# Optimization experiments

Measured on AMD Instinct MI355X. Metric: run time of the kernel, lower is better.

The kernel has to match this reference:

```python
import jax, jax.numpy as jnp
import numpy as np

D_MODEL = 1024
D_STATE = 64
D_HEAD = 64
N_HEADS = 16
D_INNER = D_HEAD * N_HEADS  # 1024
K = 4  # conv kernel size
BATCH = 4
SEQ = 4096
LN_EPS = 1e-5


def setup_inputs() -> dict:
    key = jax.random.key(0)
    k0, k1, k2, k3, k4 = jax.random.split(key, 5)
    x = jax.random.normal(k0, (BATCH, SEQ, D_MODEL), jnp.float32)
    # nn.Linear(d_model, 2*d_inner + 2*d_state, bias=False): weight (out, in)
    in_proj_w = jax.random.normal(k1, (2 * D_INNER + 2 * D_STATE, D_MODEL), jnp.float32) / np.sqrt(D_MODEL).astype(np.float32)
    # depthwise Conv1d: weight (d_inner, 1, K), bias (d_inner,)
    conv_w = jax.random.normal(k2, (D_INNER, 1, K), jnp.float32) * 0.5
    conv_b = jax.random.normal(k3, (D_INNER,), jnp.float32) * 0.1
    # _init_parameters: A = -log(arange(1..d_state)) broadcast to (H, Dh, N)
    A_param = jnp.broadcast_to(-jnp.log(jnp.arange(1, D_STATE + 1, dtype=jnp.float32))[None, None, :],
                               (N_HEADS, D_HEAD, D_STATE))
    ln_w = jnp.ones((D_INNER,), jnp.float32)
    ln_b = jnp.zeros((D_INNER,), jnp.float32)
    out_proj_w = jax.random.normal(k4, (D_MODEL, D_INNER), jnp.float32) / np.sqrt(D_INNER).astype(np.float32)
    return {"x": x, "in_proj_w": in_proj_w, "conv_w": conv_w, "conv_b": conv_b,
            "A_param": A_param, "ln_w": ln_w, "ln_b": ln_b, "out_proj_w": out_proj_w}


def _ssd_scan(xh, Bm, Cm, A_param):
    # xh: (B, L, H, Dh); Bm, Cm: (B, L, N)
    A_disc = jnp.exp(-jnp.exp(A_param))  # (H, Dh, N)

    def step(h, inp):
        x_t, B_t, C_t = inp  # (B,H,Dh), (B,N), (B,N)
        h = h * A_disc + B_t[:, None, None, :] * x_t[..., None]  # (B,H,Dh,N)
        y_t = jnp.einsum('bhdn,bn->bhd', h, C_t)
        return h, y_t

    b = xh.shape[0]
    h0 = jnp.zeros((b, N_HEADS, D_HEAD, D_STATE), xh.dtype)
    xs = (jnp.swapaxes(xh, 0, 1), jnp.swapaxes(Bm, 0, 1), jnp.swapaxes(Cm, 0, 1))
    _, ys = jax.lax.scan(step, h0, xs)  # ys: (L, B, H, Dh)
    return jnp.swapaxes(ys, 0, 1)  # (B, L, H, Dh)


def reference(x, in_proj_w, conv_w, conv_b, A_param, ln_w, ln_b, out_proj_w):
    b, L, _ = x.shape
    xBC = x @ in_proj_w.T  # (B, L, 2*d_inner + 2*d_state)
    xc = xBC[..., :D_INNER]
    z = xBC[..., D_INNER:2 * D_INNER]
    Bm = xBC[..., 2 * D_INNER:2 * D_INNER + D_STATE]
    Cm = xBC[..., 2 * D_INNER + D_STATE:]
    # causal depthwise conv (padding=3 then truncate == left-pad K-1)
    xt = jnp.swapaxes(xc, 1, 2)  # (B, C, L)
    y = jax.lax.conv_general_dilated(xt, conv_w, window_strides=(1,), padding=[(K - 1, 0)],
                                     feature_group_count=D_INNER,
                                     dimension_numbers=('NCH', 'OIH', 'NCH'))
    xc = jnp.swapaxes(y + conv_b[None, :, None], 1, 2)  # (B, L, d_inner)
    xc = jax.nn.silu(xc)
    xh = xc.reshape(b, L, N_HEADS, D_HEAD)
    yssd = _ssd_scan(xh, Bm, Cm, A_param).reshape(b, L, D_INNER)
    yg = yssd * jax.nn.silu(z)
    mu = yg.mean(-1, keepdims=True)
    var = yg.var(-1, keepdims=True)
    yn = (yg - mu) / jnp.sqrt(var + LN_EPS) * ln_w + ln_b
    return yn @ out_proj_w.T
```

## Files before the change

### kernel.cpp

```cpp
#include <hip/hip_runtime.h>

typedef unsigned short u16;
typedef unsigned int u32;
typedef __attribute__((ext_vector_type(8))) short bf16x8;
typedef __attribute__((ext_vector_type(4))) float f32x4;

#define BATCH 4
#define SEQ 4096
#define DMODEL 1024
#define DINNER 1024
#define NPROJ 2176
#define MROWS (BATCH*SEQ)
#define NCHUNK 64
#define CLEN 64
#define NPAD 2304

__device__ __forceinline__ float bf2f(u16 u) {
    union { u32 i; float f; } v; v.i = ((u32)u) << 16; return v.f;
}
__device__ __forceinline__ u16 f2bf(float f) {
    union { float f; u32 i; } v; v.f = f;
    u32 r = v.i + 0x7FFFu + ((v.i >> 16) & 1u);
    return (u16)(r >> 16);
}
__device__ __forceinline__ float silu_f(float x) { return x / (1.0f + expf(-x)); }

__device__ __forceinline__ void gload8f(const u16* p, float* o) {
    bf16x8 v = *(const bf16x8*)p;
    #pragma unroll
    for (int j = 0; j < 8; ++j) o[j] = bf2f((u16)v[j]);
}

__device__ __forceinline__ void ld_lds16(const u16* g, u16* l) {
    __builtin_amdgcn_global_load_lds(
        (const __attribute__((address_space(1))) u32*)g,
        (__attribute__((address_space(3))) u32*)l, 16, 0, 0);
}

__global__ __launch_bounds__(256) void cast_f2b(
    const float* __restrict__ src, u16* __restrict__ dst, int n8)
{
    int i = blockIdx.x * 256 + threadIdx.x;
    if (i >= n8) return;
    size_t o = (size_t)i * 8;
    float4 a = *(const float4*)(src + o);
    float4 b = *(const float4*)(src + o + 4);
    u16 v[8] = {f2bf(a.x), f2bf(a.y), f2bf(a.z), f2bf(a.w),
                f2bf(b.x), f2bf(b.y), f2bf(b.z), f2bf(b.w)};
    *(bf16x8*)(dst + o) = *(bf16x8*)v;
}

__global__ __launch_bounds__(256) void cast_w1p_k(
    const float* __restrict__ src, u16* __restrict__ dst)
{
    int i = blockIdx.x * 256 + threadIdx.x;
    int row = i >> 7;
    size_t o = (size_t)i * 8;
    u16 v[8];
    if (row < NPROJ) {
        float4 a = *(const float4*)(src + o);
        float4 b = *(const float4*)(src + o + 4);
        v[0]=f2bf(a.x); v[1]=f2bf(a.y); v[2]=f2bf(a.z); v[3]=f2bf(a.w);
        v[4]=f2bf(b.x); v[5]=f2bf(b.y); v[6]=f2bf(b.z); v[7]=f2bf(b.w);
    } else {
        #pragma unroll
        for (int j = 0; j < 8; ++j) v[j] = 0;
    }
    *(bf16x8*)(dst + o) = *(bf16x8*)v;
}

__global__ __launch_bounds__(256) void tables_k(
    const float* __restrict__ A_param, float* __restrict__ l2a_g,
    float* __restrict__ apw, float* __restrict__ ainv)
{
    __shared__ float l2s[64];
    int tid = threadIdx.x;
    if (tid < 64) {
        float v = -expf(A_param[tid]) * 1.44269504088896340736f;
        l2s[tid] = v;
        l2a_g[tid] = v;
    }
    __syncthreads();
    #pragma unroll
    for (int i = 0; i < 16; ++i) {
        int e = tid * 16 + i;
        int t = e >> 6, n = e & 63;
        float x = (float)t * l2s[n];
        apw[e]  = exp2f(x);
        ainv[e] = exp2f(-x);
    }
}

#define GK 1024
#define GNT 16

template<typename TO, int GN, int NV, int LDC>
__global__ __launch_bounds__(512, 1) void gemm8p_k(
    const u16* __restrict__ A, const u16* __restrict__ B, TO* __restrict__ C)
{
    __shared__ u16 lds[65536];

    const int cpx = (GN * 64) >> 3;
    const int bid = blockIdx.x;
    const int swz = (bid & 7) * cpx + (bid >> 3);
    const int bm = swz / GN, bn = swz % GN;
    const int m0 = bm * 256, n0 = bn * 256;

    const int tid = threadIdx.x;
    const int wid = tid >> 6, lane = tid & 63;
    const int wm = wid >> 2, wn = wid & 3;
    const int quad = lane >> 4, l16 = lane & 15;
    const int xsw = (l16 & 7) << 3;

    u16* L = lds;
    const u16* Ab = A + (size_t)m0 * GK;
    const u16* Bb = B + (size_t)n0 * GK;

    auto stage = [&](const u16* gbase, u16* ldsb) {
        {
            int c = tid;
            int row = c >> 3, slot = (c & 7) ^ (row & 7);
            ld_lds16(gbase + (size_t)row * GK + slot * 8,
                     ldsb + ((tid & ~63) << 3));
        }
        {
            int c = 512 + tid;
            int row = c >> 3, slot = (c & 7) ^ (row & 7);
            ld_lds16(gbase + (size_t)row * GK + slot * 8,
                     ldsb + ((512 + (tid & ~63)) << 3));
        }
    };
    auto rdfrag = [&](const u16* base, int rh, int kh) -> bf16x8 {
        return *(const bf16x8*)(base + rh * 64 + ((kh * 32 + quad * 8) ^ xsw));
    };

    bf16x8 aLo[4][2], aHi[4][2], bLo[2][2], bHi[2][2];
    f32x4 acc[8][4] = {};

    stage(Ab,                     L);
    stage(Ab + 128 * GK,          L + 8192);
    stage(Bb,                     L + 32768);
    stage(Bb + 128 * GK,          L + 40960);
    stage(Ab + 64,                L + 16384);
    stage(Ab + 128 * GK + 64,     L + 24576);
    asm volatile("s_waitcnt vmcnt(4)" ::: "memory");
    __builtin_amdgcn_s_barrier();
    {
        const u16* Ard = L + wm * 8192;
        #pragma unroll
        for (int i = 0; i < 4; ++i)
            #pragma unroll
            for (int kh = 0; kh < 2; ++kh)
                aLo[i][kh] = rdfrag(Ard, i * 16 + l16, kh);
    }

    for (int t = 0; t < GNT; ++t) {
        const int cb = t & 1;
        u16* Acur = L + cb * 16384;
        u16* Anxt = L + (cb ^ 1) * 16384;
        u16* Bnxt = L + 32768 + (cb ^ 1) * 16384;
        const u16* ArdC = Acur + wm * 8192;
        const u16* ArdN = Anxt + wm * 8192;
        const u16* BrdC = L + 32768 + cb * 16384 + (wn >> 1) * 8192;
        const int brh = (wn & 1) * 64;

        #pragma unroll
        for (int j = 0; j < 2; ++j)
            #pragma unroll
            for (int kh = 0; kh < 2; ++kh)
                bLo[j][kh] = rdfrag(BrdC, brh + j * 16 + l16, kh);
        if (t + 1 < GNT) stage(Bb + (t + 1) * 64, Bnxt);
        __builtin_amdgcn_s_barrier();
        asm volatile("s_waitcnt lgkmcnt(0)" ::: "memory");
        __builtin_amdgcn_s_setprio(1);
        #pragma unroll
        for (int kh = 0; kh < 2; ++kh)
            #pragma unroll
            for (int i = 0; i < 4; ++i)
                #pragma unroll
                for (int j = 0; j < 2; ++j)
                    acc[i][j] = __builtin_amdgcn_mfma_f32_16x16x32_bf16(
                        aLo[i][kh], bLo[j][kh], acc[i][j], 0, 0, 0);
        __builtin_amdgcn_s_setprio(0);
        __builtin_amdgcn_s_barrier();

        #pragma unroll
        for (int j = 0; j < 2; ++j)
            #pragma unroll
            for (int kh = 0; kh < 2; ++kh)
                bHi[j][kh] = rdfrag(BrdC, brh + 32 + j * 16 + l16, kh);
        if (t + 1 < GNT) stage(Bb + 128 * GK + (t + 1) * 64, Bnxt + 8192);
        __builtin_amdgcn_s_barrier();
        asm volatile("s_waitcnt lgkmcnt(0)" ::: "memory");
        __builtin_amdgcn_s_setprio(1);
        #pragma unroll
        for (int kh = 0; kh < 2; ++kh)
            #pragma unroll
            for (int i = 0; i < 4; ++i)
                #pragma unroll
                for (int j = 0; j < 2; ++j)
                    acc[i][2 + j] = __builtin_amdgcn_mfma_f32_16x16x32_bf16(
                        aLo[i][kh], bHi[j][kh], acc[i][2 + j], 0, 0, 0);
        __builtin_amdgcn_s_setprio(0);
        __builtin_amdgcn_s_barrier();

        #pragma unroll
        for (int i = 0; i < 4; ++i)
            #pragma unroll
            for (int kh = 0; kh < 2; ++kh)
                aHi[i][kh] = rdfrag(ArdC, 64 + i * 16 + l16, kh);
        if (t + 2 < GNT) stage(Ab + (t + 2) * 64, Acur);
        if (t + 2 < GNT)      { asm volatile("s_waitcnt vmcnt(6)" ::: "memory"); }
        else if (t + 1 < GNT) { asm volatile("s_waitcnt vmcnt(4)" ::: "memory"); }
        __builtin_amdgcn_s_barrier();
        asm volatile("s_waitcnt lgkmcnt(0)" ::: "memory");
        __builtin_amdgcn_s_setprio(1);
        #pragma unroll
        for (int kh = 0; kh < 2; ++kh)
            #pragma unroll
            for (int i = 0; i < 4; ++i)
                #pragma unroll
                for (int j = 0; j < 2; ++j)
                    acc[4 + i][2 + j] = __builtin_amdgcn_mfma_f32_16x16x32_bf16(
                        aHi[i][kh], bHi[j][kh], acc[4 + i][2 + j], 0, 0, 0);
        __builtin_amdgcn_s_setprio(0);
        __builtin_amdgcn_s_barrier();

        if (t + 1 < GNT) {
            #pragma unroll
            for (int i = 0; i < 4; ++i)
                #pragma unroll
                for (int kh = 0; kh < 2; ++kh)
                    aLo[i][kh] = rdfrag(ArdN, i * 16 + l16, kh);
        }
        if (t + 2 < GNT) stage(Ab + 128 * GK + (t + 2) * 64, Acur + 8192);
        if (t + 2 < GNT)      { asm volatile("s_waitcnt vmcnt(4)" ::: "memory"); }
        else if (t + 1 < GNT) { asm volatile("s_waitcnt vmcnt(0)" ::: "memory"); }
        __builtin_amdgcn_s_barrier();
        asm volatile("s_waitcnt lgkmcnt(0)" ::: "memory");
        __builtin_amdgcn_s_setprio(1);
        #pragma unroll
        for (int kh = 0; kh < 2; ++kh)
            #pragma unroll
            for (int i = 0; i < 4; ++i)
                #pragma unroll
                for (int j = 0; j < 2; ++j)
                    acc[4 + i][j] = __builtin_amdgcn_mfma_f32_16x16x32_bf16(
                        aHi[i][kh], bLo[j][kh], acc[4 + i][j], 0, 0, 0);
        __builtin_amdgcn_s_setprio(0);
        __builtin_amdgcn_s_barrier();
    }

    __syncthreads();
    if constexpr (sizeof(TO) == 2) {
        u16* eld = lds;
        #pragma unroll
        for (int i = 0; i < 8; ++i)
            #pragma unroll
            for (int j = 0; j < 4; ++j)
                #pragma unroll
                for (int r = 0; r < 4; ++r)
                    eld[(size_t)(wm * 128 + i * 16 + quad * 4 + r) * 256 +
                        wn * 64 + j * 16 + l16] = f2bf(acc[i][j][r]);
        __syncthreads();
        #pragma unroll
        for (int rep = 0; rep < 16; ++rep) {
            int cc = rep * 512 + tid;
            int row = cc >> 5, c8 = (cc & 31) * 8;
            if (n0 + c8 < NV)
                *(bf16x8*)(C + (size_t)(m0 + row) * LDC + n0 + c8) =
                    *(const bf16x8*)(eld + (size_t)row * 256 + c8);
        }
    } else {
        float* eldf = (float*)lds;
        #pragma unroll
        for (int h = 0; h < 2; ++h) {
            if (wm == h) {
                #pragma unroll
                for (int i = 0; i < 8; ++i)
                    #pragma unroll
                    for (int j = 0; j < 4; ++j)
                        #pragma unroll
                        for (int r = 0; r < 4; ++r)
                            eldf[(size_t)(i * 16 + quad * 4 + r) * 256 +
                                 wn * 64 + j * 16 + l16] = acc[i][j][r];
            }
            __syncthreads();
            #pragma unroll
            for (int rep = 0; rep < 16; ++rep) {
                int cc = rep * 512 + tid;
                int row = cc >> 6, c4 = (cc & 63) * 4;
                *(float4*)(C + (size_t)(m0 + h * 128 + row) * LDC + n0 + c4) =
                    *(const float4*)(eldf + (size_t)row * 256 + c4);
            }
            __syncthreads();
        }
    }
}

__global__ __launch_bounds__(256) void ssd_intra_k(
    const float* __restrict__ conv_w, const float* __restrict__ conv_b,
    const u16* __restrict__ xBC, u16* __restrict__ yout,
    u16* __restrict__ Sh, const float* __restrict__ apw,
    const float* __restrict__ ainv)
{
    __shared__ u16 Pl[64][72];
    __shared__ u16 Ql[64][72];
    __shared__ u16 Gl[64][72];
    __shared__ u16 Qt[64][72];
    __shared__ u16 Xt[64][72];

    const int dg = blockIdx.x, c = blockIdx.y, b = blockIdx.z;
    const int dcol = dg * 64;
    const int l0 = c * CLEN;
    const int tid = threadIdx.x;
    const int w = tid >> 6, lane = tid & 63;
    const int quad = lane >> 4, l16 = lane & 15;
    const int tstrip = 16 * w;

    {
        const int st_t = tid >> 3, st_n8 = (tid & 7) * 8;
        #pragma unroll
        for (int rep = 0; rep < 2; ++rep) {
            int t = rep * 32 + st_t;
            size_t row = (size_t)(b * SEQ + l0 + t) * NPROJ;
            float Bv[8], Cv[8];
            gload8f(xBC + row + 2048 + st_n8, Bv);
            gload8f(xBC + row + 2112 + st_n8, Cv);
            float4 aw0 = *(const float4*)&apw[t * 64 + st_n8];
            float4 aw1 = *(const float4*)&apw[t * 64 + st_n8 + 4];
            float4 ai0 = *(const float4*)&ainv[t * 64 + st_n8];
            float4 ai1 = *(const float4*)&ainv[t * 64 + st_n8 + 4];
            float4 ar0 = *(const float4*)&apw[(63 - t) * 64 + st_n8];
            float4 ar1 = *(const float4*)&apw[(63 - t) * 64 + st_n8 + 4];
            float aw[8] = {aw0.x,aw0.y,aw0.z,aw0.w,aw1.x,aw1.y,aw1.z,aw1.w};
            float ai[8] = {ai0.x,ai0.y,ai0.z,ai0.w,ai1.x,ai1.y,ai1.z,ai1.w};
            float ar[8] = {ar0.x,ar0.y,ar0.z,ar0.w,ar1.x,ar1.y,ar1.z,ar1.w};
            u16 p8[8], q8[8];
            #pragma unroll
            for (int j = 0; j < 8; ++j) {
                p8[j] = f2bf(Cv[j] * aw[j]);
                q8[j] = f2bf(Bv[j] * ai[j]);
            }
            *(bf16x8*)&Pl[t][st_n8] = *(bf16x8*)p8;
            *(bf16x8*)&Ql[t][st_n8] = *(bf16x8*)q8;
            #pragma unroll
            for (int j = 0; j < 8; ++j)
                Qt[st_n8 + j][t] = f2bf(Bv[j] * ar[j]);
        }
    }
    {
        const int xt_d8 = (tid & 7) * 8;
        const int ch0 = dcol + xt_d8;
        float4 wv[8];
        #pragma unroll
        for (int j = 0; j < 8; ++j)
            wv[j] = *(const float4*)(conv_w + (ch0 + j) * 4);
        float bias[8];
        {
            float4 b0 = *(const float4*)(conv_b + ch0);
            float4 b1 = *(const float4*)(conv_b + ch0 + 4);
            bias[0]=b0.x; bias[1]=b0.y; bias[2]=b0.z; bias[3]=b0.w;
            bias[4]=b1.x; bias[5]=b1.y; bias[6]=b1.z; bias[7]=b1.w;
        }
        #pragma unroll
        for (int rep = 0; rep < 2; ++rep) {
            int xt_t = (tid >> 3) + rep * 32;
            float acc[8];
            #pragma unroll
            for (int j = 0; j < 8; ++j) acc[j] = bias[j];
            #pragma unroll
            for (int k = 0; k < 4; ++k) {
                int lt = l0 + xt_t - 3 + k;
                if (lt < 0) continue;
                float v[8];
                gload8f(xBC + (size_t)(b * SEQ + lt) * NPROJ + ch0, v);
                #pragma unroll
                for (int j = 0; j < 8; ++j) {
                    const float* wj = (const float*)&wv[j];
                    acc[j] += v[j] * wj[k];
                }
            }
            #pragma unroll
            for (int j = 0; j < 8; ++j)
                Xt[xt_d8 + j][xt_t] = f2bf(silu_f(acc[j]));
        }
    }
    __syncthreads();

    bf16x8 af0 = *(const bf16x8*)&Pl[tstrip + l16][0  + quad * 8];
    bf16x8 af1 = *(const bf16x8*)&Pl[tstrip + l16][32 + quad * 8];
    f32x4 g[4] = {};
    #pragma unroll
    for (int j4 = 0; j4 < 4; ++j4) {
        bf16x8 b0 = *(const bf16x8*)&Ql[j4 * 16 + l16][0  + quad * 8];
        bf16x8 b1 = *(const bf16x8*)&Ql[j4 * 16 + l16][32 + quad * 8];
        g[j4] = __builtin_amdgcn_mfma_f32_16x16x32_bf16(af0, b0, g[j4], 0, 0, 0);
        g[j4] = __builtin_amdgcn_mfma_f32_16x16x32_bf16(af1, b1, g[j4], 0, 0, 0);
    }
    __syncthreads();

    #pragma unroll
    for (int j4 = 0; j4 < 4; ++j4) {
        #pragma unroll
        for (int r = 0; r < 4; ++r) {
            int t = tstrip + quad * 4 + r;
            int s = j4 * 16 + l16;
            float val = (s <= t) ? g[j4][r] : 0.f;
            u16 hi = f2bf(val);
            Ql[t][s] = hi;
            Gl[t][s] = f2bf(val - bf2f(hi));
        }
    }
    __syncthreads();

    bf16x8 gh0 = *(const bf16x8*)&Ql[tstrip + l16][0  + quad * 8];
    bf16x8 gh1 = *(const bf16x8*)&Ql[tstrip + l16][32 + quad * 8];
    bf16x8 gl0 = *(const bf16x8*)&Gl[tstrip + l16][0  + quad * 8];
    bf16x8 gl1 = *(const bf16x8*)&Gl[tstrip + l16][32 + quad * 8];
    bf16x8 qt0 = *(const bf16x8*)&Qt[tstrip + l16][0  + quad * 8];
    bf16x8 qt1 = *(const bf16x8*)&Qt[tstrip + l16][32 + quad * 8];

    #pragma unroll
    for (int dt = 0; dt < 4; ++dt) {
        bf16x8 x0 = *(const bf16x8*)&Xt[dt * 16 + l16][0  + quad * 8];
        bf16x8 x1 = *(const bf16x8*)&Xt[dt * 16 + l16][32 + quad * 8];
        f32x4 y = {};
        y = __builtin_amdgcn_mfma_f32_16x16x32_bf16(gh0, x0, y, 0, 0, 0);
        y = __builtin_amdgcn_mfma_f32_16x16x32_bf16(gh1, x1, y, 0, 0, 0);
        y = __builtin_amdgcn_mfma_f32_16x16x32_bf16(gl0, x0, y, 0, 0, 0);
        y = __builtin_amdgcn_mfma_f32_16x16x32_bf16(gl1, x1, y, 0, 0, 0);
        f32x4 s4 = {};
        s4 = __builtin_amdgcn_mfma_f32_16x16x32_bf16(qt0, x0, s4, 0, 0, 0);
        s4 = __builtin_amdgcn_mfma_f32_16x16x32_bf16(qt1, x1, s4, 0, 0, 0);
        #pragma unroll
        for (int r = 0; r < 4; ++r) {
            int t = tstrip + quad * 4 + r;
            yout[(size_t)(b * SEQ + l0 + t) * DINNER + dcol + dt * 16 + l16] = f2bf(y[r]);
            int n = tstrip + quad * 4 + r;
            Sh[((size_t)((b * NCHUNK + c) * 64 + n)) * 1024 + dcol + dt * 16 + l16] = f2bf(s4[r]);
        }
    }
}

__global__ __launch_bounds__(256) void state_scan_k(
    u16* __restrict__ Sh, const float* __restrict__ l2a)
{
    int gid = blockIdx.x * 256 + threadIdx.x;
    int b = gid >> 16, r = gid & 65535, n = r >> 10;
    float a64 = exp2f(64.f * l2a[n]);
    float v = 0.f;
    size_t base = ((size_t)b << 22) + r;
    for (int c = 0; c < NCHUNK; ++c) {
        size_t addr = base + ((size_t)c << 16);
        float s = bf2f(Sh[addr]);
        Sh[addr] = f2bf(v);
        v = fmaf(v, a64, s);
    }
}

__global__ __launch_bounds__(256) void ssd_inter_k(
    u16* __restrict__ Y, const u16* __restrict__ xBC,
    const u16* __restrict__ Sh, const float* __restrict__ apw,
    const float* __restrict__ l2a)
{
    __shared__ u16 Pl[64][72];
    __shared__ u16 Vt[64][72];

    const int dg = blockIdx.x, c = blockIdx.y, b = blockIdx.z;
    const int dcol = dg * 64;
    const int l0 = c * CLEN;
    const int tid = threadIdx.x;
    const int w = tid >> 6, lane = tid & 63;
    const int quad = lane >> 4, l16 = lane & 15;
    const int tstrip = 16 * w;

    {
        const int st_t = tid >> 3, st_n8 = (tid & 7) * 8;
        #pragma unroll
        for (int rep = 0; rep < 2; ++rep) {
            int t = rep * 32 + st_t;
            float Cv[8];
            gload8f(xBC + (size_t)(b * SEQ + l0 + t) * NPROJ + 2112 + st_n8, Cv);
            float4 aw0 = *(const float4*)&apw[t * 64 + st_n8];
            float4 aw1 = *(const float4*)&apw[t * 64 + st_n8 + 4];
            float aw[8] = {aw0.x,aw0.y,aw0.z,aw0.w,aw1.x,aw1.y,aw1.z,aw1.w};
            u16 p8[8];
            #pragma unroll
            for (int j = 0; j < 8; ++j) p8[j] = f2bf(Cv[j] * aw[j]);
            *(bf16x8*)&Pl[t][st_n8] = *(bf16x8*)p8;
        }
    }
    {
        #pragma unroll
        for (int rep = 0; rep < 2; ++rep) {
            int idx = rep * 256 + tid;
            int vn = idx >> 3, vd8 = (idx & 7) * 8;
            float an = exp2f(l2a[vn]);
            bf16x8 vv = *(const bf16x8*)&Sh[((size_t)((b * NCHUNK + c) * 64 + vn)) * 1024 + dcol + vd8];
            #pragma unroll
            for (int j = 0; j < 8; ++j) Vt[vd8 + j][vn] = f2bf(an * bf2f((u16)vv[j]));
        }
    }
    __syncthreads();

    bf16x8 af0 = *(const bf16x8*)&Pl[tstrip + l16][0  + quad * 8];
    bf16x8 af1 = *(const bf16x8*)&Pl[tstrip + l16][32 + quad * 8];
    #pragma unroll
    for (int dt = 0; dt < 4; ++dt) {
        bf16x8 hb0 = *(const bf16x8*)&Vt[dt * 16 + l16][0  + quad * 8];
        bf16x8 hb1 = *(const bf16x8*)&Vt[dt * 16 + l16][32 + quad * 8];
        f32x4 y = {};
        y = __builtin_amdgcn_mfma_f32_16x16x32_bf16(af0, hb0, y, 0, 0, 0);
        y = __builtin_amdgcn_mfma_f32_16x16x32_bf16(af1, hb1, y, 0, 0, 0);
        #pragma unroll
        for (int r = 0; r < 4; ++r) {
            int t = tstrip + quad * 4 + r;
            size_t addr = (size_t)(b * SEQ + l0 + t) * DINNER + dcol + dt * 16 + l16;
            Y[addr] = f2bf(bf2f(Y[addr]) + y[r]);
        }
    }
}

__global__ __launch_bounds__(256) void gate_k(
    const u16* __restrict__ Y, const u16* __restrict__ xBC,
    const float* __restrict__ ln_w, const float* __restrict__ ln_b,
    u16* __restrict__ yn)
{
    __shared__ float r1[4], r2[4];
    const int row = blockIdx.x;
    const int tid = threadIdx.x;
    const int lane = tid & 63, wid = tid >> 6;

    float gv[4];
    {
        const ushort4 yv = *(const ushort4*)(Y + (size_t)row * DINNER + tid * 4);
        const ushort4 zv = *(const ushort4*)(xBC + (size_t)row * NPROJ + 1024 + tid * 4);
        gv[0] = bf2f(yv.x) * silu_f(bf2f(zv.x));
        gv[1] = bf2f(yv.y) * silu_f(bf2f(zv.y));
        gv[2] = bf2f(yv.z) * silu_f(bf2f(zv.z));
        gv[3] = bf2f(yv.w) * silu_f(bf2f(zv.w));
    }
    float ps = gv[0] + gv[1] + gv[2] + gv[3];
    float pq = gv[0]*gv[0] + gv[1]*gv[1] + gv[2]*gv[2] + gv[3]*gv[3];
    #pragma unroll
    for (int off = 1; off < 64; off <<= 1) {
        ps += __shfl_xor(ps, off);
        pq += __shfl_xor(pq, off);
    }
    if (lane == 0) { r1[wid] = ps; r2[wid] = pq; }
    __syncthreads();
    float ts = r1[0] + r1[1] + r1[2] + r1[3];
    float tq = r2[0] + r2[1] + r2[2] + r2[3];
    float mu = ts * (1.0f / DINNER);
    float var = tq * (1.0f / DINNER) - mu * mu;
    float inv = rsqrtf(var + 1e-5f);

    u16 outv[4];
    #pragma unroll
    for (int j = 0; j < 4; ++j) {
        int c = tid * 4 + j;
        float v = (gv[j] - mu) * inv * ln_w[c] + ln_b[c];
        outv[j] = f2bf(v);
    }
    *(ushort4*)(yn + (size_t)row * DINNER + tid * 4) = *(ushort4*)outv;
}

extern "C" void kernel_launch(void* const* d_in, const int* in_sizes, int n_in,
                              void* d_out, int out_size, void* d_ws, size_t ws_size,
                              hipStream_t stream) {
    const float* x   = (const float*)d_in[0];
    const float* w1  = (const float*)d_in[1];
    const float* cw  = (const float*)d_in[2];
    const float* cb  = (const float*)d_in[3];
    const float* ap  = (const float*)d_in[4];
    const float* lnw = (const float*)d_in[5];
    const float* lnb = (const float*)d_in[6];
    const float* w2  = (const float*)d_in[7];
    float* out = (float*)d_out;

    u16* xBC   = (u16*)d_ws;
    u16* xact  = xBC + (size_t)MROWS * NPROJ;
    u16* x_bf  = xact;
    u16* w2_bf = xact + (size_t)MROWS * DINNER;
    float* l2a  = (float*)(w2_bf + (size_t)DMODEL * DINNER);
    float* apw  = l2a + 64;
    float* ainv = apw + 4096;
    u16* w1p = (u16*)d_out;
    u16* Sh  = (u16*)d_out;

    cast_f2b<<<(MROWS * DMODEL / 8) / 256, 256, 0, stream>>>(x, x_bf, MROWS * DMODEL / 8);
    cast_w1p_k<<<(NPAD * DMODEL / 8) / 256, 256, 0, stream>>>(w1, w1p);
    cast_f2b<<<(DMODEL * DINNER / 8) / 256, 256, 0, stream>>>(w2, w2_bf, DMODEL * DINNER / 8);
    tables_k<<<1, 256, 0, stream>>>(ap, l2a, apw, ainv);

    gemm8p_k<u16, 9, NPROJ, NPROJ><<<9 * 64, 512, 0, stream>>>(x_bf, w1p, xBC);

    ssd_intra_k<<<dim3(16, NCHUNK, BATCH), 256, 0, stream>>>(cw, cb, xBC, xact, Sh, apw, ainv);
    state_scan_k<<<1024, 256, 0, stream>>>(Sh, l2a);
    ssd_inter_k<<<dim3(16, NCHUNK, BATCH), 256, 0, stream>>>(xact, xBC, Sh, apw, l2a);

    gate_k<<<MROWS, 256, 0, stream>>>(xact, xBC, lnw, lnb, xact);
    gemm8p_k<float, 4, DMODEL, DMODEL><<<4 * 64, 512, 0, stream>>>(xact, w2_bf, out);
}
```

Measured before the change: 383.6 us.

## Use 256x128-tile in-projection GEMM to avoid padding N to 2304

Adds a dedicated in-projection GEMM kernel with 256x128 output tiles, so N=2176 divides into 17 column tiles and no padded columns are computed. The padded weight cast kernel is dropped in favor of the plain cast over the real 2176 rows. It keeps a double-buffered LDS pipeline with direct global-to-LDS loads and an LDS-staged bf16 epilogue. The change removes wasted MFMA work on the padding and rebalances the grid to 1088 blocks, at the cost of lower per-block arithmetic intensity, since each A tile is reused across fewer columns.

```diff
diff --git a/kernel.cpp b/kernel.cpp
--- a/kernel.cpp
+++ b/kernel.cpp
@@ -13,7 +13,6 @@
 #define MROWS (BATCH*SEQ)
 #define NCHUNK 64
 #define CLEN 64
-#define NPAD 2304
 
 __device__ __forceinline__ float bf2f(u16 u) {
     union { u32 i; float f; } v; v.i = ((u32)u) << 16; return v.f;
@@ -50,25 +49,6 @@
     *(bf16x8*)(dst + o) = *(bf16x8*)v;
 }
 
-__global__ __launch_bounds__(256) void cast_w1p_k(
-    const float* __restrict__ src, u16* __restrict__ dst)
-{
-    int i = blockIdx.x * 256 + threadIdx.x;
-    int row = i >> 7;
-    size_t o = (size_t)i * 8;
-    u16 v[8];
-    if (row < NPROJ) {
-        float4 a = *(const float4*)(src + o);
-        float4 b = *(const float4*)(src + o + 4);
-        v[0]=f2bf(a.x); v[1]=f2bf(a.y); v[2]=f2bf(a.z); v[3]=f2bf(a.w);
-        v[4]=f2bf(b.x); v[5]=f2bf(b.y); v[6]=f2bf(b.z); v[7]=f2bf(b.w);
-    } else {
-        #pragma unroll
-        for (int j = 0; j < 8; ++j) v[j] = 0;
-    }
-    *(bf16x8*)(dst + o) = *(bf16x8*)v;
-}
-
 __global__ __launch_bounds__(256) void tables_k(
     const float* __restrict__ A_param, float* __restrict__ l2a_g,
     float* __restrict__ apw, float* __restrict__ ainv)
@@ -93,6 +73,177 @@
 
 #define GK 1024
 #define GNT 16
+
+#define G1N 17
+__global__ __launch_bounds__(512, 1) void gemm1_k(
+    const u16* __restrict__ A, const u16* __restrict__ B, u16* __restrict__ C)
+{
+    __shared__ u16 lds[49152];
+
+    const int bid = blockIdx.x;
+    const int swz = (bid & 7) * 136 + (bid >> 3);
+    const int bm = swz / G1N, bn = swz % G1N;
+    const int m0 = bm * 256, n0 = bn * 128;
+
+    const int tid = threadIdx.x;
+    const int wid = tid >> 6, lane = tid & 63;
+    const int wm = wid >> 2, wn = wid & 3;
+    const int quad = lane >> 4, l16 = lane & 15;
+    const int xsw = (l16 & 7) << 3;
+
+    u16* L = lds;
+    const u16* Ab = A + (size_t)m0 * GK;
+    const u16* Bb = B + (size_t)n0 * GK;
+
+    auto stage_a = [&](const u16* gbase, u16* ldsb) {
+        {
+            int c = tid;
+            int row = c >> 3, slot = (c & 7) ^ (row & 7);
+            ld_lds16(gbase + (size_t)row * GK + slot * 8,
+                     ldsb + ((tid & ~63) << 3));
+        }
+        {
+            int c = 512 + tid;
+            int row = c >> 3, slot = (c & 7) ^ (row & 7);
+            ld_lds16(gbase + (size_t)row * GK + slot * 8,
+                     ldsb + ((512 + (tid & ~63)) << 3));
+        }
+    };
+    auto stage_b = [&](const u16* gbase, u16* ldsb) {
+        int row = tid >> 3, slot = (tid & 7) ^ (row & 7);
+        ld_lds16(gbase + (size_t)row * GK + slot * 8,
+                 ldsb + ((tid & ~63) << 3));
+    };
+    auto rdfrag = [&](const u16* base, int rh, int kh) -> bf16x8 {
+        return *(const bf16x8*)(base + rh * 64 + ((kh * 32 + quad * 8) ^ xsw));
+    };
+
+    bf16x8 aLo[4][2], aHi[4][2], bLo[2], bHi[2];
+    f32x4 acc[8][2] = {};
+
+    stage_a(Ab,                  L);
+    stage_a(Ab + 128 * GK,       L + 8192);
+    stage_b(Bb,                  L + 32768);
+    stage_b(Bb + 64 * GK,        L + 36864);
+    stage_a(Ab + 64,             L + 16384);
+    stage_a(Ab + 128 * GK + 64,  L + 24576);
+    asm volatile("s_waitcnt vmcnt(4)" ::: "memory");
+    __builtin_amdgcn_s_barrier();
+    {
+        const u16* Ard = L + wm * 8192;
+        #pragma unroll
+        for (int i = 0; i < 4; ++i)
+            #pragma unroll
+            for (int kh = 0; kh < 2; ++kh)
+                aLo[i][kh] = rdfrag(Ard, i * 16 + l16, kh);
+    }
+
+    for (int t = 0; t < GNT; ++t) {
+        const int cb = t & 1;
+        u16* Acur = L + cb * 16384;
+        u16* Anxt = L + (cb ^ 1) * 16384;
+        u16* Bnxt = L + 32768 + (cb ^ 1) * 8192;
+        const u16* ArdC = Acur + wm * 8192;
+        const u16* ArdN = Anxt + wm * 8192;
+        const u16* BrdC = L + 32768 + cb * 8192 + (wn >> 1) * 4096;
+        const int brh = (wn & 1) * 32;
+
+        #pragma unroll
+        for (int kh = 0; kh < 2; ++kh)
+            bLo[kh] = rdfrag(BrdC, brh + l16, kh);
+        if (t + 1 < GNT) stage_b(Bb + (t + 1) * 64, Bnxt);
+        __builtin_amdgcn_s_barrier();
+        asm volatile("s_waitcnt lgkmcnt(0)" ::: "memory");
+        __builtin_amdgcn_s_setprio(1);
+        #pragma unroll
+        for (int kh = 0; kh < 2; ++kh)
+            #pragma unroll
+            for (int i = 0; i < 4; ++i)
+                acc[i][0] = __builtin_amdgcn_mfma_f32_16x16x32_bf16(
+                    aLo[i][kh], bLo[kh], acc[i][0], 0, 0, 0);
+        __builtin_amdgcn_s_setprio(0);
+        __builtin_amdgcn_s_barrier();
+
+        #pragma unroll
+        for (int kh = 0; kh < 2; ++kh)
+            bHi[kh] = rdfrag(BrdC, brh + 16 + l16, kh);
+        if (t + 1 < GNT) stage_b(Bb + 64 * GK + (t + 1) * 64, Bnxt + 4096);
+        __builtin_amdgcn_s_barrier();
+        asm volatile("s_waitcnt lgkmcnt(0)" ::: "memory");
+        __builtin_amdgcn_s_setprio(1);
+        #pragma unroll
+        for (int kh = 0; kh < 2; ++kh)
+            #pragma unroll
+            for (int i = 0; i < 4; ++i)
+                acc[i][1] = __builtin_amdgcn_mfma_f32_16x16x32_bf16(
+                    aLo[i][kh], bHi[kh], acc[i][1], 0, 0, 0);
+        __builtin_amdgcn_s_setprio(0);
+        __builtin_amdgcn_s_barrier();
+
+        #pragma unroll
+        for (int i = 0; i < 4; ++i)
+            #pragma unroll
+            for (int kh = 0; kh < 2; ++kh)
+                aHi[i][kh] = rdfrag(ArdC, 64 + i * 16 + l16, kh);
+        if (t + 2 < GNT) stage_a(Ab + (t + 2) * 64, Acur);
+        if (t + 2 < GNT)      { asm volatile("s_waitcnt vmcnt(4)" ::: "memory"); }
+        else if (t + 1 < GNT) { asm volatile("s_waitcnt vmcnt(2)" ::: "memory"); }
+        __builtin_amdgcn_s_barrier();
+        asm volatile("s_waitcnt lgkmcnt(0)" ::: "memory");
+        __builtin_amdgcn_s_setprio(1);
+        #pragma unroll
+        for (int kh = 0; kh < 2; ++kh)
+            #pragma unroll
+            for (int i = 0; i < 4; ++i)
+                acc[4 + i][1] = __builtin_amdgcn_mfma_f32_16x16x32_bf16(
+                    aHi[i][kh], bHi[kh], acc[4 + i][1], 0, 0, 0);
+        __builtin_amdgcn_s_setprio(0);
+        __builtin_amdgcn_s_barrier();
+
+        if (t + 1 < GNT) {
+            #pragma unroll
+            for (int i = 0; i < 4; ++i)
+                #pragma unroll
+                for (int kh = 0; kh < 2; ++kh)
+                    aLo[i][kh] = rdfrag(ArdN, i * 16 + l16, kh);
+        }
+        if (t + 2 < GNT) stage_a(Ab + 128 * GK + (t + 2) * 64, Acur + 8192);
+        if (t + 2 < GNT)      { asm volatile("s_waitcnt vmcnt(4)" ::: "memory"); }
+        else if (t + 1 < GNT) { asm volatile("s_waitcnt vmcnt(0)" ::: "memory"); }
+        __builtin_amdgcn_s_barrier();
+        asm volatile("s_waitcnt lgkmcnt(0)" ::: "memory");
+        __builtin_amdgcn_s_setprio(1);
+        #pragma unroll
+        for (int kh = 0; kh < 2; ++kh)
+            #pragma unroll
+            for (int i = 0; i < 4; ++i)
+                acc[4 + i][0] = __builtin_amdgcn_mfma_f32_16x16x32_bf16(
+                    aHi[i][kh], bLo[kh], acc[4 + i][0], 0, 0, 0);
+        __builtin_amdgcn_s_setprio(0);
+        __builtin_amdgcn_s_barrier();
+    }
+
+    __syncthreads();
+    {
+        u16* eld = lds;
+        #pragma unroll
+        for (int i = 0; i < 8; ++i)
+            #pragma unroll
+            for (int j = 0; j < 2; ++j)
+                #pragma unroll
+                for (int r = 0; r < 4; ++r)
+                    eld[(size_t)(wm * 128 + i * 16 + quad * 4 + r) * 128 +
+                        wn * 32 + j * 16 + l16] = f2bf(acc[i][j][r]);
+        __syncthreads();
+        #pragma unroll
+        for (int rep = 0; rep < 8; ++rep) {
+            int cc = rep * 512 + tid;
+            int row = cc >> 4, c8 = (cc & 15) * 8;
+            *(bf16x8*)(C + (size_t)(m0 + row) * NPROJ + n0 + c8) =
+                *(const bf16x8*)(eld + (size_t)row * 128 + c8);
+        }
+    }
+}
 
 template<typename TO, int GN, int NV, int LDC>
 __global__ __launch_bounds__(512, 1) void gemm8p_k(
@@ -586,15 +737,15 @@
     float* l2a  = (float*)(w2_bf + (size_t)DMODEL * DINNER);
     float* apw  = l2a + 64;
     float* ainv = apw + 4096;
-    u16* w1p = (u16*)d_out;
-    u16* Sh  = (u16*)d_out;
+    u16* w1_bf = (u16*)d_out;
+    u16* Sh    = (u16*)d_out;
 
     cast_f2b<<<(MROWS * DMODEL / 8) / 256, 256, 0, stream>>>(x, x_bf, MROWS * DMODEL / 8);
-    cast_w1p_k<<<(NPAD * DMODEL / 8) / 256, 256, 0, stream>>>(w1, w1p);
+    cast_f2b<<<(NPROJ * DMODEL / 8) / 256, 256, 0, stream>>>(w1, w1_bf, NPROJ * DMODEL / 8);
     cast_f2b<<<(DMODEL * DINNER / 8) / 256, 256, 0, stream>>>(w2, w2_bf, DMODEL * DINNER / 8);
     tables_k<<<1, 256, 0, stream>>>(ap, l2a, apw, ainv);
 
-    gemm8p_k<u16, 9, NPROJ, NPROJ><<<9 * 64, 512, 0, stream>>>(x_bf, w1p, xBC);
+    gemm1_k<<<64 * G1N, 512, 0, stream>>>(x_bf, w1_bf, xBC);
 
     ssd_intra_k<<<dim3(16, NCHUNK, BATCH), 256, 0, stream>>>(cw, cb, xBC, xact, Sh, apw, ainv);
     state_scan_k<<<1024, 256, 0, stream>>>(Sh, l2a);
```

Result: no change. 388.3 us (+1.2%).

## Replace in-projection GEMM with BK=32 double-buffered kernel using less LDS

Applied to the files above, without the earlier changes.

Adds a new in-projection GEMM kernel that uses a K-tile of 32 and 64KB of LDS instead of 128KB, and launch bounds that request up to 4 blocks per SM. It splits each K step into four quadrant MFMA phases and interleaves the global-to-LDS staging of the next B tile and the A tile two steps ahead, with barriers and priority bumps between phases. The aim is better occupancy and better overlap of memory traffic with MFMA work. The cost is twice as many K iterations, each with many barriers, plus register pressure from the 128 accumulators at the higher occupancy target.

```diff
diff --git a/kernel.cpp b/kernel.cpp
--- a/kernel.cpp
+++ b/kernel.cpp
@@ -92,6 +92,165 @@
 }
 
 #define GK 1024
+
+#define GNT32 32
+__global__ __launch_bounds__(512, 4) void gemm1bk32_k(
+    const u16* __restrict__ A, const u16* __restrict__ B, u16* __restrict__ C)
+{
+    __shared__ u16 lds[32768];
+
+    const int bid = blockIdx.x;
+    const int swz = (bid & 7) * 72 + (bid >> 3);
+    const int bm = swz / 9, bn = swz % 9;
+    const int m0 = bm * 256, n0 = bn * 256;
+
+    const int tid = threadIdx.x;
+    const int wid = tid >> 6, lane = tid & 63;
+    const int wm = wid >> 2, wn = wid & 3;
+    const int quad = lane >> 4, l16 = lane & 15;
+    const int s32 = (quad ^ ((l16 >> 1) & 3)) * 8;
+
+    u16* L = lds;
+    const u16* Ab = A + (size_t)m0 * GK;
+    const u16* Bb = B + (size_t)n0 * GK;
+
+    auto stage = [&](const u16* gbase, u16* ldsb) {
+        int row = tid >> 2, slot = (tid & 3) ^ ((row >> 1) & 3);
+        ld_lds16(gbase + (size_t)row * GK + slot * 8,
+                 ldsb + ((tid & ~63) << 3));
+    };
+    auto rdfrag = [&](const u16* base, int rh) -> bf16x8 {
+        return *(const bf16x8*)(base + rh * 32 + s32);
+    };
+
+    bf16x8 aLo[4], aHi[4], bLo[2], bHi[2];
+    f32x4 acc[8][4] = {};
+
+    stage(Ab,                 L);
+    stage(Ab + 128 * GK,      L + 4096);
+    stage(Bb,                 L + 16384);
+    stage(Bb + 128 * GK,      L + 20480);
+    stage(Ab + 32,            L + 8192);
+    stage(Ab + 128 * GK + 32, L + 12288);
+    asm volatile("s_waitcnt vmcnt(2)" ::: "memory");
+    __builtin_amdgcn_s_barrier();
+    {
+        const u16* Ard = L + wm * 4096;
+        #pragma unroll
+        for (int i = 0; i < 4; ++i)
+            aLo[i] = rdfrag(Ard, i * 16 + l16);
+    }
+
+    for (int t = 0; t < GNT32; ++t) {
+        const int cb = t & 1;
+        u16* Acur = L + cb * 8192;
+        u16* Anxt = L + (cb ^ 1) * 8192;
+        u16* Bnxt = L + 16384 + (cb ^ 1) * 8192;
+        const u16* ArdC = Acur + wm * 4096;
+        const u16* ArdN = Anxt + wm * 4096;
+        const u16* BrdC = L + 16384 + cb * 8192 + (wn >> 1) * 4096;
+        const int brh = (wn & 1) * 64;
+
+        #pragma unroll
+        for (int j = 0; j < 2; ++j)
+            bLo[j] = rdfrag(BrdC, brh + j * 16 + l16);
+        if (t + 1 < GNT32) stage(Bb + (t + 1) * 32, Bnxt);
+        __builtin_amdgcn_s_barrier();
+        asm volatile("s_waitcnt lgkmcnt(0)" ::: "memory");
+        __builtin_amdgcn_s_setprio(1);
+        #pragma unroll
+        for (int i = 0; i < 4; ++i)
+            #pragma unroll
+            for (int j = 0; j < 2; ++j)
+                acc[i][j] = __builtin_amdgcn_mfma_f32_16x16x32_bf16(
+                    aLo[i], bLo[j], acc[i][j], 0, 0, 0);
+        __builtin_amdgcn_s_setprio(0);
+        __builtin_amdgcn_s_barrier();
+
+        #pragma unroll
+        for (int j = 0; j < 2; ++j)
+            bHi[j] = rdfrag(BrdC, brh + 32 + j * 16 + l16);
+        if (t + 1 < GNT32) stage(Bb + 128 * GK + (t + 1) * 32, Bnxt + 4096);
+        __builtin_amdgcn_s_barrier();
+        asm volatile("s_waitcnt lgkmcnt(0)" ::: "memory");
+        __builtin_amdgcn_s_setprio(1);
+        #pragma unroll
+        for (int i = 0; i < 4; ++i)
+            #pragma unroll
+            for (int j = 0; j < 2; ++j)
+                acc[i][2 + j] = __builtin_amdgcn_mfma_f32_16x16x32_bf16(
+                    aLo[i], bHi[j], acc[i][2 + j], 0, 0, 0);
+        __builtin_amdgcn_s_setprio(0);
+        __builtin_amdgcn_s_barrier();
+
+        #pragma unroll
+        for (int i = 0; i < 4; ++i)
+            aHi[i] = rdfrag(ArdC, 64 + i * 16 + l16);
+        if (t + 2 < GNT32) stage(Ab + (t + 2) * 32, Acur);
+        if (t + 2 < GNT32)      { asm volatile("s_waitcnt vmcnt(3)" ::: "memory"); }
+        else if (t + 1 < GNT32) { asm volatile("s_waitcnt vmcnt(2)" ::: "memory"); }
+        __builtin_amdgcn_s_barrier();
+        asm volatile("s_waitcnt lgkmcnt(0)" ::: "memory");
+        __builtin_amdgcn_s_setprio(1);
+        #pragma unroll
+        for (int i = 0; i < 4; ++i)
+            #pragma unroll
+            for (int j = 0; j < 2; ++j)
+                acc[4 + i][2 + j] = __builtin_amdgcn_mfma_f32_16x16x32_bf16(
+                    aHi[i], bHi[j], acc[4 + i][2 + j], 0, 0, 0);
+        __builtin_amdgcn_s_setprio(0);
+        __builtin_amdgcn_s_barrier();
+
+        if (t + 1 < GNT32) {
+            #pragma unroll
+            for (int i = 0; i < 4; ++i)
+                aLo[i] = rdfrag(ArdN, i * 16 + l16);
+        }
+        if (t + 2 < GNT32) stage(Ab + 128 * GK + (t + 2) * 32, Acur + 4096);
+        if (t + 2 < GNT32)      { asm volatile("s_waitcnt vmcnt(2)" ::: "memory"); }
+        else if (t + 1 < GNT32) { asm volatile("s_waitcnt vmcnt(0)" ::: "memory"); }
+        __builtin_amdgcn_s_barrier();
+        asm volatile("s_waitcnt lgkmcnt(0)" ::: "memory");
+        __builtin_amdgcn_s_setprio(1);
+        #pragma unroll
+        for (int i = 0; i < 4; ++i)
+            #pragma unroll
+            for (int j = 0; j < 2; ++j)
+                acc[4 + i][j] = __builtin_amdgcn_mfma_f32_16x16x32_bf16(
+                    aHi[i], bLo[j], acc[4 + i][j], 0, 0, 0);
+        __builtin_amdgcn_s_setprio(0);
+        __builtin_amdgcn_s_barrier();
+    }
+
+    __syncthreads();
+    {
+        u16* eld = lds;
+        #pragma unroll
+        for (int h = 0; h < 2; ++h) {
+            if (wm == h) {
+                #pragma unroll
+                for (int i = 0; i < 8; ++i)
+                    #pragma unroll
+                    for (int j = 0; j < 4; ++j)
+                        #pragma unroll
+                        for (int r = 0; r < 4; ++r)
+                            eld[(size_t)(i * 16 + quad * 4 + r) * 256 +
+                                wn * 64 + j * 16 + l16] = f2bf(acc[i][j][r]);
+            }
+            __syncthreads();
+            #pragma unroll
+            for (int rep = 0; rep < 8; ++rep) {
+                int cc = rep * 512 + tid;
+                int row = cc >> 5, c8 = (cc & 31) * 8;
+                if (n0 + c8 < NPROJ)
+                    *(bf16x8*)(C + (size_t)(m0 + h * 128 + row) * NPROJ + n0 + c8) =
+                        *(const bf16x8*)(eld + (size_t)row * 256 + c8);
+            }
+            __syncthreads();
+        }
+    }
+}
+
 #define GNT 16
 
 template<typename TO, int GN, int NV, int LDC>
@@ -594,7 +753,7 @@
     cast_f2b<<<(DMODEL * DINNER / 8) / 256, 256, 0, stream>>>(w2, w2_bf, DMODEL * DINNER / 8);
     tables_k<<<1, 256, 0, stream>>>(ap, l2a, apw, ainv);
 
-    gemm8p_k<u16, 9, NPROJ, NPROJ><<<9 * 64, 512, 0, stream>>>(x_bf, w1p, xBC);
+    gemm1bk32_k<<<9 * 64, 512, 0, stream>>>(x_bf, w1p, xBC);
 
     ssd_intra_k<<<dim3(16, NCHUNK, BATCH), 256, 0, stream>>>(cw, cb, xBC, xact, Sh, apw, ainv);
     state_scan_k<<<1024, 256, 0, stream>>>(Sh, l2a);
```

Result: slower. 1.300 ms (+239.0%).
